# Performance work log

Hardware: AMD Instinct MI355X
Metric: run time of the kernel (lower is better)

Reference implementation:

```python
import jax, jax.numpy as jnp
import numpy as np

N, T, D_MODEL, H, DK = 4, 4096, 1024, 16, 64


def setup_inputs() -> dict:
    key = jax.random.key(0)
    ks = jax.random.split(key, 16)
    randn = lambda k, sh: jax.random.normal(k, sh, dtype=jnp.float32)
    # linear weights stored (in, out) so y = x @ W + b (math-equivalent to torch Linear)
    scale = 1.0 / np.sqrt(D_MODEL)
    return {
        "x_k": randn(ks[0], (N, T, D_MODEL)),
        "x_v": randn(ks[1], (N, T, D_MODEL)),
        "x_q": randn(ks[2], (N, T, D_MODEL)),
        "mask": jnp.ones((N, T), dtype=jnp.int32),
        "Wk": randn(ks[3], (D_MODEL, H * DK)) * scale,
        "bk": randn(ks[4], (H * DK,)) * 0.02,
        "Wv": randn(ks[5], (D_MODEL, H * DK)) * scale,
        "bv": randn(ks[6], (H * DK,)) * 0.02,
        "Wq": randn(ks[7], (D_MODEL, H * DK)) * scale,
        "bq": randn(ks[8], (H * DK,)) * 0.02,
        "alpha_w": randn(ks[9], (DK,)),
        "beta_w": randn(ks[10], (DK,)),
        "Wr": randn(ks[11], (DK, DK)) * (1.0 / np.sqrt(DK)),
        "br": randn(ks[12], (DK,)) * 0.02,
        "Wfc": randn(ks[13], (H * DK, D_MODEL)) * scale,
        "bfc": randn(ks[14], (D_MODEL,)) * 0.02,
    }


def _split_heads(x):  # (n, t, h*d) -> (n, h, t, d)
    n, t, _ = x.shape
    return x.reshape(n, t, H, DK).transpose(0, 2, 1, 3)


def reference(x_k, x_v, x_q, mask, Wk, bk, Wv, bv, Wq, bq,
              alpha_w, beta_w, Wr, br, Wfc, bfc):
    scale = DK ** (-0.5)
    k = _split_heads(x_k @ Wk + bk)  # (n, h, t, d)
    v = _split_heads(x_v @ Wv + bv)
    q = _split_heads(x_q @ Wq + bq)

    m = (mask == 0)[:, None, :]  # (n, 1, t) True where masked
    neg_inf = jnp.finfo(q.dtype).min

    # alpha pooling over queries -> global query (n, h, d)
    alpha = jnp.einsum('nhtd,d->nht', q, alpha_w) * scale
    alpha = jnp.where(m, neg_inf, alpha)
    alpha = jax.nn.softmax(alpha, axis=-1)
    global_query = jnp.einsum('nht,nhtd->nhd', alpha, q)

    # p = broadcast(global_query) * k, then beta pooling -> global key
    p = global_query[:, :, None, :] * k  # (n, h, t, d)
    beta = jnp.einsum('nhtd,d->nht', p, beta_w) * scale
    beta = jnp.where(m, neg_inf, beta)
    beta = jax.nn.softmax(beta, axis=-1)
    global_key = jnp.einsum('nht,nhtd->nhd', beta, p)

    u = global_key[:, :, None, :] * v  # (n, h, t, d)
    u_r = u @ Wr + br
    A = u_r + q  # (n, h, t, d)
    A = A.transpose(0, 2, 1, 3).reshape(N, T, H * DK)
    return A @ Wfc + bfc
```

## Files before the change

### kernel.cpp

```cpp
#include <hip/hip_runtime.h>

typedef __bf16 bf16x8 __attribute__((ext_vector_type(8)));
typedef float f32x4 __attribute__((ext_vector_type(4)));
typedef unsigned int u32x4 __attribute__((ext_vector_type(4)));
typedef unsigned short u16x4 __attribute__((ext_vector_type(4)));
typedef unsigned short u16x8 __attribute__((ext_vector_type(8)));

#define SEQ_T 4096
#define DMODEL 1024
#define HEADS 16
#define DKH 64
#define MTOK 16384

#define AS1 __attribute__((address_space(1)))
#define AS3 __attribute__((address_space(3)))

__device__ __forceinline__ unsigned short f2bf(float f) {
  unsigned u = __builtin_bit_cast(unsigned int, f);
  u += 0x7FFFu + ((u >> 16) & 1u);
  return (unsigned short)(u >> 16);
}
__device__ __forceinline__ float bf2f(unsigned short h) {
  unsigned u = ((unsigned)h) << 16;
  return __builtin_bit_cast(float, u);
}
__device__ __forceinline__ void gload16(const unsigned short* g, unsigned short* l) {
  __builtin_amdgcn_global_load_lds((const AS1 unsigned int*)(g),
                                   (AS3 unsigned int*)(l), 16, 0, 0);
}

__global__ void __launch_bounds__(256) k_cvt(const float* __restrict__ x,
                                             unsigned short* __restrict__ y,
                                             long long nelem) {
  long long i = ((long long)blockIdx.x * 256 + threadIdx.x) * 8;
  if (i >= nelem) return;
  u16x8 o;
#pragma unroll
  for (int j = 0; j < 8; ++j) o[j] = f2bf(x[i + j]);
  *(u16x8*)(y + i) = o;
}

__global__ void __launch_bounds__(256) k_wtrans(const float* __restrict__ W,
                                                unsigned short* __restrict__ Wt,
                                                int K, int N) {
  __shared__ float tile[32][33];
  int bn = blockIdx.x * 32, bk = blockIdx.y * 32;
  int tx = threadIdx.x, ty = threadIdx.y;
#pragma unroll
  for (int j = 0; j < 32; j += 8)
    tile[ty + j][tx] = W[(size_t)(bk + ty + j) * N + bn + tx];
  __syncthreads();
#pragma unroll
  for (int j = 0; j < 32; j += 8)
    Wt[(size_t)(bn + ty + j) * K + bk + tx] = f2bf(tile[tx][ty + j]);
}

#define BM 128
#define BN 128
#define BK 64

template <int OBF, int SCORE, int FUSEA>
__global__ void __launch_bounds__(256, 2)
k_gemm(const unsigned short* __restrict__ A, const unsigned short* __restrict__ Bt,
       const float* __restrict__ bias, void* __restrict__ C,
       const int* __restrict__ mask, const float* __restrict__ swt,
       float* __restrict__ sbuf, const unsigned short* __restrict__ qadd,
       int M, int N, int K) {
  __shared__ unsigned short As[BM * BK];
  __shared__ unsigned short Bs[BN * BK];
  const int tid = threadIdx.x;
  const int lane = tid & 63, wid = tid >> 6;
  const int wr = wid >> 1, wc = wid & 1;
  const int bnb = blockIdx.x;
  const int bm = blockIdx.y * BM, bn = bnb * BN;
  const int l15 = lane & 15, l4 = lane >> 4;

  const unsigned short* Btn = FUSEA ? Bt + ((size_t)(bm >> 12) << 20) : Bt;
  const float* biasn = FUSEA ? bias + ((bm >> 12) << 10) : bias;

  f32x4 acc[4][4];
#pragma unroll
  for (int i = 0; i < 4; ++i)
#pragma unroll
    for (int j = 0; j < 4; ++j)
#pragma unroll
      for (int e = 0; e < 4; ++e) acc[i][j][e] = 0.f;

  const int sgr = lane >> 3;
  const int sgc = (lane & 7) ^ sgr;

  for (int kt = 0; kt < K; kt += BK) {
    __syncthreads();
#pragma unroll
    for (int j = 0; j < 4; ++j) {
      int rb = wid * 32 + j * 8;
      gload16(A + (size_t)(bm + rb + sgr) * K + kt + sgc * 8, As + rb * BK);
    }
#pragma unroll
    for (int j = 0; j < 4; ++j) {
      int rb = wid * 32 + j * 8;
      gload16(Btn + (size_t)(bn + rb + sgr) * K + kt + sgc * 8, Bs + rb * BK);
    }
    __syncthreads();
#pragma unroll
    for (int kh = 0; kh < 2; ++kh) {
      bf16x8 af[4], bfr[4];
#pragma unroll
      for (int m = 0; m < 4; ++m) {
        int ra = wr * 64 + m * 16 + l15;
        int sl = (kh * 4 + l4) ^ (ra & 7);
        af[m] = *(const bf16x8*)(As + ra * BK + sl * 8);
      }
#pragma unroll
      for (int n = 0; n < 4; ++n) {
        int rb = wc * 64 + n * 16 + l15;
        int sl = (kh * 4 + l4) ^ (rb & 7);
        bfr[n] = *(const bf16x8*)(Bs + rb * BK + sl * 8);
      }
#pragma unroll
      for (int m = 0; m < 4; ++m)
#pragma unroll
        for (int n = 0; n < 4; ++n)
          acc[m][n] = __builtin_amdgcn_mfma_f32_16x16x32_bf16(af[m], bfr[n],
                                                              acc[m][n], 0, 0, 0);
    }
  }

  const int crow = bm + wr * 64 + l4 * 4;
  const int ccol = bn + wc * 64 + l15;

  float pacc[4][4];
  const float* wrow = nullptr;
  if (SCORE == 1) wrow = swt;
  if (SCORE) {
#pragma unroll
    for (int m = 0; m < 4; ++m)
#pragma unroll
      for (int e = 0; e < 4; ++e) pacc[m][e] = 0.f;
  }

#pragma unroll
  for (int m = 0; m < 4; ++m)
#pragma unroll
    for (int n = 0; n < 4; ++n) {
      int c = ccol + n * 16;
      float bj = biasn[c];
      float wg = SCORE ? wrow[n * 16 + l15] : 0.f;
#pragma unroll
      for (int e = 0; e < 4; ++e) {
        int r = crow + m * 16 + e;
        float v = acc[m][n][e] + bj;
        if (FUSEA) v += bf2f(qadd[(size_t)r * N + c]);
        if (SCORE) pacc[m][e] += v * wg;
        if (OBF)
          ((unsigned short*)C)[(size_t)r * N + c] = f2bf(v);
        else
          ((float*)C)[(size_t)r * N + c] = v;
      }
    }

  if (SCORE) {
#pragma unroll
    for (int m = 0; m < 4; ++m)
#pragma unroll
      for (int e = 0; e < 4; ++e) {
        float p = pacc[m][e];
        p += __shfl_xor(p, 1);
        p += __shfl_xor(p, 2);
        p += __shfl_xor(p, 4);
        p += __shfl_xor(p, 8);
        if (l15 == 0) {
          int r = crow + m * 16 + e;
          int t = r & (SEQ_T - 1), n = r >> 12;
          float sc = p * 0.125f;
          if (mask[n * SEQ_T + t] == 0) sc = -3.0e38f;
          sbuf[((size_t)n * HEADS + bnb * 2 + wc) * SEQ_T + t] = sc;
        }
      }
  }
}

__global__ void __launch_bounds__(256) k_softmax(const float* __restrict__ s,
                                                 float* __restrict__ mxo,
                                                 float* __restrict__ invo) {
  __shared__ float red[4];
  const int tid = threadIdx.x, lane = tid & 63, wid = tid >> 6;
  const float* sb = s + (size_t)blockIdx.x * SEQ_T;
  float m = -3.4e38f;
  for (int t = tid; t < SEQ_T; t += 256) m = fmaxf(m, sb[t]);
#pragma unroll
  for (int o = 1; o < 64; o <<= 1) m = fmaxf(m, __shfl_xor(m, o));
  if (lane == 0) red[wid] = m;
  __syncthreads();
  m = fmaxf(fmaxf(red[0], red[1]), fmaxf(red[2], red[3]));
  __syncthreads();
  float sum = 0.f;
  for (int t = tid; t < SEQ_T; t += 256) sum += __expf(sb[t] - m);
#pragma unroll
  for (int o = 1; o < 64; o <<= 1) sum += __shfl_xor(sum, o);
  if (lane == 0) red[wid] = sum;
  __syncthreads();
  if (tid == 0) {
    mxo[blockIdx.x] = m;
    invo[blockIdx.x] = 1.f / (red[0] + red[1] + red[2] + red[3]);
  }
}

__global__ void __launch_bounds__(256) k_wsum(const unsigned short* __restrict__ X,
                                              const float* __restrict__ s,
                                              const float* __restrict__ mxv,
                                              const float* __restrict__ invv,
                                              float* __restrict__ pbuf) {
  __shared__ float part[16][64];
  const int nh = blockIdx.x >> 4, chunk = blockIdx.x & 15;
  const int n = nh >> 4, h = nh & 15;
  const int tid = threadIdx.x, lane = tid & 63, wid = tid >> 6;
  const int tsub = lane >> 4, dl = lane & 15;
  const float mx = mxv[nh], inv = invv[nh];
  const float* sb = s + (size_t)nh * SEQ_T + chunk * 256;
  const size_t base = ((size_t)n * SEQ_T + chunk * 256) * DMODEL + h * DKH + dl * 4;
  f32x4 acc = {0.f, 0.f, 0.f, 0.f};
  for (int t = wid * 4 + tsub; t < 256; t += 16) {
    float w = __expf(sb[t] - mx) * inv;
    u16x4 xv = *(const u16x4*)(X + base + (size_t)t * DMODEL);
    acc[0] += w * bf2f(xv[0]);
    acc[1] += w * bf2f(xv[1]);
    acc[2] += w * bf2f(xv[2]);
    acc[3] += w * bf2f(xv[3]);
  }
  int g = wid * 4 + tsub;
#pragma unroll
  for (int e = 0; e < 4; ++e) part[g][dl * 4 + e] = acc[e];
  __syncthreads();
  if (tid < 64) {
    float v = 0.f;
#pragma unroll
    for (int gg = 0; gg < 16; ++gg) v += part[gg][tid];
    pbuf[(size_t)blockIdx.x * 64 + tid] = v;
  }
}

__global__ void __launch_bounds__(64) k_fin(const float* __restrict__ pbuf,
                                            const float* __restrict__ bw,
                                            float* __restrict__ out,
                                            float* __restrict__ wv) {
  const int nh = blockIdx.x, d = threadIdx.x;
  float v = 0.f;
#pragma unroll
  for (int c = 0; c < 16; ++c) v += pbuf[((size_t)nh * 16 + c) * 64 + d];
  out[(size_t)nh * 64 + d] = v;
  wv[(size_t)nh * 64 + d] = v * bw[d];
}

__global__ void __launch_bounds__(256) k_wksb(const float* __restrict__ Wk,
                                              const float* __restrict__ bk,
                                              const float* __restrict__ wv,
                                              unsigned short* __restrict__ WksT,
                                              float* __restrict__ bks) {
  const int nh = blockIdx.x, tid = threadIdx.x;
  const int n = nh >> 4, h = nh & 15;
  __shared__ float wvs[64];
  if (tid < 64) wvs[tid] = wv[(size_t)nh * 64 + tid];
  __syncthreads();
  int c0 = tid * 4;
  u16x4 o;
#pragma unroll
  for (int i = 0; i < 4; ++i) {
    int c = c0 + i;
    const float* wr = Wk + (size_t)c * DMODEL + h * DKH;
    float acc = 0.f;
#pragma unroll
    for (int dd = 0; dd < 64; dd += 4) {
      f32x4 w4 = *(const f32x4*)(wr + dd);
      acc += w4[0] * wvs[dd] + w4[1] * wvs[dd + 1] + w4[2] * wvs[dd + 2] +
             w4[3] * wvs[dd + 3];
    }
    o[i] = f2bf(acc);
  }
  *(u16x4*)(WksT + (size_t)n * 16 * DMODEL + (size_t)h * DMODEL + c0) = o;
  if (tid < 64) {
    float p = bk[h * 64 + tid] * wvs[tid];
#pragma unroll
    for (int ofs = 1; ofs < 64; ofs <<= 1) p += __shfl_xor(p, ofs);
    if (tid == 0) bks[nh] = p;
  }
}

__global__ void __launch_bounds__(128) k_score(const unsigned short* __restrict__ xk,
                                               const unsigned short* __restrict__ WksT,
                                               const float* __restrict__ bks,
                                               const int* __restrict__ mask,
                                               float* __restrict__ sbuf) {
  __shared__ unsigned short Xs[64 * 32];
  __shared__ unsigned short Ws[16 * 32];
  const int tid = threadIdx.x, lane = tid & 63, wid = tid >> 6;
  const int l15 = lane & 15, l4 = lane >> 4;
  const int bm = blockIdx.x * 64;
  const int n = bm >> 12;
  const unsigned short* Wn = WksT + (size_t)n * 16 * DMODEL;

  f32x4 acc[2];
#pragma unroll
  for (int m = 0; m < 2; ++m)
#pragma unroll
    for (int e = 0; e < 4; ++e) acc[m][e] = 0.f;

  const int srow = lane >> 2, scol = (lane & 3) * 8;
  for (int kt = 0; kt < DMODEL; kt += 32) {
    __syncthreads();
#pragma unroll
    for (int j = 0; j < 2; ++j) {
      int rb = wid * 32 + j * 16;
      gload16(xk + (size_t)(bm + rb + srow) * DMODEL + kt + scol, Xs + rb * 32);
    }
    if (wid == 0) gload16(Wn + (size_t)srow * DMODEL + kt + scol, Ws);
    __syncthreads();
    bf16x8 bfr = *(const bf16x8*)(Ws + l15 * 32 + l4 * 8);
#pragma unroll
    for (int m = 0; m < 2; ++m) {
      bf16x8 af = *(const bf16x8*)(Xs + (wid * 32 + m * 16 + l15) * 32 + l4 * 8);
      acc[m] = __builtin_amdgcn_mfma_f32_16x16x32_bf16(af, bfr, acc[m], 0, 0, 0);
    }
  }
  const int h = l15;
  const float bh = bks[n * 16 + h];
#pragma unroll
  for (int m = 0; m < 2; ++m)
#pragma unroll
    for (int e = 0; e < 4; ++e) {
      int r = bm + wid * 32 + m * 16 + l4 * 4 + e;
      int t = r & (SEQ_T - 1);
      float sc = (acc[m][e] + bh) * 0.125f;
      if (mask[n * SEQ_T + t] == 0) sc = -3.0e38f;
      sbuf[((size_t)n * HEADS + h) * SEQ_T + t] = sc;
    }
}

__global__ void __launch_bounds__(256) k_bwsum(const unsigned short* __restrict__ xk,
                                               const float* __restrict__ s,
                                               const float* __restrict__ smx,
                                               const float* __restrict__ sinv,
                                               float* __restrict__ part) {
  __shared__ float eb[16][64];
  const int tc = blockIdx.x, n = blockIdx.y, tid = threadIdx.x;
#pragma unroll
  for (int i = 0; i < 4; ++i) {
    int idx = i * 256 + tid;
    int h = idx >> 6, t = idx & 63;
    int nh = n * 16 + h;
    eb[h][t] = __expf(s[(size_t)nh * SEQ_T + tc * 64 + t] - smx[nh]) * sinv[nh];
  }
  __syncthreads();
  const int c0 = tid * 4;
  f32x4 acc[16];
#pragma unroll
  for (int h = 0; h < 16; ++h)
#pragma unroll
    for (int e = 0; e < 4; ++e) acc[h][e] = 0.f;
  const unsigned short* xb = xk + ((size_t)n * SEQ_T + tc * 64) * DMODEL + c0;
  for (int t = 0; t < 64; ++t) {
    u16x4 xr = *(const u16x4*)(xb + (size_t)t * DMODEL);
    float x0 = bf2f(xr[0]), x1 = bf2f(xr[1]), x2 = bf2f(xr[2]), x3 = bf2f(xr[3]);
#pragma unroll
    for (int h = 0; h < 16; ++h) {
      float w = eb[h][t];
      acc[h][0] += w * x0;
      acc[h][1] += w * x1;
      acc[h][2] += w * x2;
      acc[h][3] += w * x3;
    }
  }
#pragma unroll
  for (int h = 0; h < 16; ++h)
    *(f32x4*)(part + (((size_t)(n * 64 + tc)) * 16 + h) * DMODEL + c0) = acc[h];
}

__global__ void __launch_bounds__(256) k_gkr(const float* __restrict__ part,
                                             const unsigned short* __restrict__ WkT,
                                             const float* __restrict__ bk,
                                             const float* __restrict__ gq,
                                             float* __restrict__ gk) {
  __shared__ float pl[DMODEL];
  const int nh = blockIdx.x, tid = threadIdx.x;
  const int n = nh >> 4, h = nh & 15;
  const int c0 = tid * 4;
  f32x4 a4 = {0.f, 0.f, 0.f, 0.f};
  for (int tc = 0; tc < 64; ++tc) {
    f32x4 p = *(const f32x4*)(part + (((size_t)(n * 64 + tc)) * 16 + h) * DMODEL + c0);
    a4[0] += p[0]; a4[1] += p[1]; a4[2] += p[2]; a4[3] += p[3];
  }
#pragma unroll
  for (int e = 0; e < 4; ++e) pl[c0 + e] = a4[e];
  __syncthreads();
  if (tid < 64) {
    const unsigned short* wr = WkT + (size_t)(h * 64 + tid) * DMODEL;
    float acc = 0.f;
    for (int c = 0; c < DMODEL; c += 8) {
      u16x8 w = *(const u16x8*)(wr + c);
#pragma unroll
      for (int j = 0; j < 8; ++j) acc += pl[c + j] * bf2f(w[j]);
    }
    gk[(size_t)nh * 64 + tid] = gq[(size_t)nh * 64 + tid] * (acc + bk[h * 64 + tid]);
  }
}

__global__ void __launch_bounds__(256) k_wrgb(const float* __restrict__ gk,
                                              const float* __restrict__ Wr,
                                              const float* __restrict__ bv,
                                              const float* __restrict__ br,
                                              unsigned short* __restrict__ WrgT,
                                              float* __restrict__ bcomb) {
  __shared__ float wl[4096];
  const int nh = blockIdx.x, tid = threadIdx.x;
  const int n = nh >> 4, h = nh & 15;
#pragma unroll
  for (int i = 0; i < 16; ++i) {
    int idx = i * 256 + tid;
    int d = idx >> 6, dd = idx & 63;
    float v = gk[nh * 64 + dd] * Wr[dd * 64 + d];
    wl[idx] = v;
    WrgT[(size_t)nh * 4096 + idx] = f2bf(v);
  }
  __syncthreads();
  if (tid < 64) {
    float acc = br[tid];
#pragma unroll
    for (int dd = 0; dd < 64; ++dd) acc += bv[h * 64 + dd] * wl[tid * 64 + dd];
    bcomb[(size_t)n * DMODEL + h * 64 + tid] = acc;
  }
}

#define LDW 72
__global__ void __launch_bounds__(256) k_wcomb(const unsigned short* __restrict__ WrgT,
                                               const unsigned short* __restrict__ WvN,
                                               unsigned short* __restrict__ WcombT) {
  __shared__ unsigned short Wg[64 * LDW];
  __shared__ unsigned short Vv[128 * LDW];
  const int rc = blockIdx.x, nh = blockIdx.y;
  const int n = nh >> 4, h = nh & 15;
  const int tid = threadIdx.x, lane = tid & 63, wid = tid >> 6;
  const int l15 = lane & 15, l4 = lane >> 4;
#pragma unroll
  for (int i = 0; i < 2; ++i) {
    int v = i * 256 + tid;
    int d = v >> 3, k8 = v & 7;
    *(u16x8*)(Wg + d * LDW + k8 * 8) =
        *(const u16x8*)(WrgT + (size_t)nh * 4096 + d * 64 + k8 * 8);
  }
#pragma unroll
  for (int i = 0; i < 4; ++i) {
    int v = i * 256 + tid;
    int r = v >> 3, k8 = v & 7;
    *(u16x8*)(Vv + r * LDW + k8 * 8) =
        *(const u16x8*)(WvN + (size_t)(rc * 128 + r) * DMODEL + h * 64 + k8 * 8);
  }
  __syncthreads();
  f32x4 acc[8];
#pragma unroll
  for (int ct = 0; ct < 8; ++ct)
#pragma unroll
    for (int e = 0; e < 4; ++e) acc[ct][e] = 0.f;
#pragma unroll
  for (int ks = 0; ks < 2; ++ks) {
    bf16x8 af = *(const bf16x8*)(Wg + (wid * 16 + l15) * LDW + ks * 32 + l4 * 8);
#pragma unroll
    for (int ct = 0; ct < 8; ++ct) {
      bf16x8 bf = *(const bf16x8*)(Vv + (ct * 16 + l15) * LDW + ks * 32 + l4 * 8);
      acc[ct] = __builtin_amdgcn_mfma_f32_16x16x32_bf16(af, bf, acc[ct], 0, 0, 0);
    }
  }
  unsigned short* out = WcombT + ((size_t)n << 20);
#pragma unroll
  for (int ct = 0; ct < 8; ++ct)
#pragma unroll
    for (int e = 0; e < 4; ++e) {
      int d = h * 64 + wid * 16 + l4 * 4 + e;
      int r = rc * 128 + ct * 16 + l15;
      out[(size_t)d * DMODEL + r] = f2bf(acc[ct][e]);
    }
}

extern "C" void kernel_launch(void* const* d_in, const int* in_sizes, int n_in,
                              void* d_out, int out_size, void* d_ws, size_t ws_size,
                              hipStream_t stream) {
  const float* x_k = (const float*)d_in[0];
  const float* x_v = (const float*)d_in[1];
  const float* x_q = (const float*)d_in[2];
  const int* mask = (const int*)d_in[3];
  const float* Wk = (const float*)d_in[4];
  const float* bk = (const float*)d_in[5];
  const float* Wv = (const float*)d_in[6];
  const float* bv = (const float*)d_in[7];
  const float* Wq = (const float*)d_in[8];
  const float* bq = (const float*)d_in[9];
  const float* alpha_w = (const float*)d_in[10];
  const float* beta_w = (const float*)d_in[11];
  const float* Wr = (const float*)d_in[12];
  const float* br = (const float*)d_in[13];
  const float* Wfc = (const float*)d_in[14];
  const float* bfc = (const float*)d_in[15];

  unsigned short* qbf = (unsigned short*)d_out;

  char* ws = (char*)d_ws;
  const size_t MB = 1024 * 1024;
  unsigned short* xst = (unsigned short*)(ws);
  unsigned short* abuf = (unsigned short*)(ws + 32 * MB);
  unsigned short* WqT = (unsigned short*)(ws + 64 * MB);
  unsigned short* WkT = WqT + (size_t)DMODEL * DMODEL;
  unsigned short* WfT = WkT + (size_t)DMODEL * DMODEL;
  unsigned short* WvN = WfT + (size_t)DMODEL * DMODEL;
  unsigned short* WcombT = WvN + (size_t)DMODEL * DMODEL;
  unsigned short* WrgT = WcombT + (size_t)4 * DMODEL * DMODEL;
  unsigned short* WksT = WrgT + (size_t)64 * 4096;
  float* part = (float*)(WksT + (size_t)4 * 16 * DMODEL);
  float* pooled = part + (size_t)256 * 16 * DMODEL;
  float* sbuf = pooled + (size_t)64 * DMODEL;
  float* pbuf = sbuf + (size_t)64 * SEQ_T;
  float* smx = pbuf + 1024 * 64;
  float* sinv = smx + 64;
  float* gq = sinv + 64;
  float* wvb = gq + 4096;
  float* gk = wvb + 4096;
  float* bks = gk + 4096;
  float* bcomb = bks + 64;

  dim3 tb(32, 8);
  dim3 tg(DMODEL / 32, DMODEL / 32);
  k_wtrans<<<tg, tb, 0, stream>>>(Wq, WqT, DMODEL, DMODEL);
  k_wtrans<<<tg, tb, 0, stream>>>(Wk, WkT, DMODEL, DMODEL);
  k_wtrans<<<tg, tb, 0, stream>>>(Wfc, WfT, DMODEL, DMODEL);
  k_cvt<<<512, 256, 0, stream>>>(Wv, WvN, (long long)DMODEL * DMODEL);

  long long nx = (long long)MTOK * DMODEL;
  int cvtg = (int)(nx / 8 / 256);
  dim3 ggrid(DMODEL / BN, MTOK / BM);

  k_cvt<<<cvtg, 256, 0, stream>>>(x_q, xst, nx);
  k_gemm<1, 1, 0><<<ggrid, 256, 0, stream>>>(xst, WqT, bq, (void*)qbf, mask,
                                             alpha_w, sbuf, nullptr,
                                             MTOK, DMODEL, DMODEL);
  k_softmax<<<64, 256, 0, stream>>>(sbuf, smx, sinv);
  k_wsum<<<1024, 256, 0, stream>>>(qbf, sbuf, smx, sinv, pbuf);
  k_fin<<<64, 64, 0, stream>>>(pbuf, beta_w, gq, wvb);

  k_wksb<<<64, 256, 0, stream>>>(Wk, bk, wvb, WksT, bks);
  k_cvt<<<cvtg, 256, 0, stream>>>(x_k, xst, nx);
  k_score<<<MTOK / 64, 128, 0, stream>>>(xst, WksT, bks, mask, sbuf);
  k_softmax<<<64, 256, 0, stream>>>(sbuf, smx, sinv);
  dim3 bwg(64, 4);
  k_bwsum<<<bwg, 256, 0, stream>>>(xst, sbuf, smx, sinv, part);
  k_gkr<<<64, 256, 0, stream>>>(part, WkT, bk, gq, gk);

  k_wrgb<<<64, 256, 0, stream>>>(gk, Wr, bv, br, WrgT, bcomb);
  dim3 wcg(8, 64);
  k_wcomb<<<wcg, 256, 0, stream>>>(WrgT, WvN, WcombT);

  k_cvt<<<cvtg, 256, 0, stream>>>(x_v, xst, nx);
  k_gemm<1, 0, 1><<<ggrid, 256, 0, stream>>>(xst, WcombT, bcomb, (void*)abuf,
                                             nullptr, nullptr, nullptr, qbf,
                                             MTOK, DMODEL, DMODEL);

  k_gemm<0, 0, 0><<<ggrid, 256, 0, stream>>>(abuf, WfT, bfc, d_out, nullptr,
                                             nullptr, nullptr, nullptr,
                                             MTOK, DMODEL, DMODEL);
}
```

Before: 308.5 us.

## Merge input conversions, fuse tiny reduction kernels, and remap GEMM workgroup order

The three fp32-to-bf16 input conversions are merged into one launch that writes x_k into abuf and x_v into the second half of the output buffer. Two pairs of tiny kernels are fused (k_fin into k_wksb, and k_gkr with k_wrgb) so the global query and global key stay in shared memory instead of round-tripping through global memory. GEMM workgroups are remapped with a stride-8 permutation, likely to spread neighbouring tiles across XCDs for better L2 locality. The goal is fewer kernel launches and less global traffic. The cost is reusing the output buffer as scratch, which depends on the output being large enough.

```diff
diff --git a/kernel.cpp b/kernel.cpp
--- a/kernel.cpp
+++ b/kernel.cpp
@@ -34,6 +34,22 @@
                                              long long nelem) {
   long long i = ((long long)blockIdx.x * 256 + threadIdx.x) * 8;
   if (i >= nelem) return;
+  u16x8 o;
+#pragma unroll
+  for (int j = 0; j < 8; ++j) o[j] = f2bf(x[i + j]);
+  *(u16x8*)(y + i) = o;
+}
+
+__global__ void __launch_bounds__(256) k_cvt3(const float* __restrict__ xq,
+                                              const float* __restrict__ xk,
+                                              const float* __restrict__ xv,
+                                              unsigned short* __restrict__ oq,
+                                              unsigned short* __restrict__ ok,
+                                              unsigned short* __restrict__ ov) {
+  const int which = blockIdx.x >> 13;
+  const float* x = which == 0 ? xq : (which == 1 ? xk : xv);
+  unsigned short* y = which == 0 ? oq : (which == 1 ? ok : ov);
+  long long i = ((long long)(blockIdx.x & 8191) * 256 + threadIdx.x) * 8;
   u16x8 o;
 #pragma unroll
   for (int j = 0; j < 8; ++j) o[j] = f2bf(x[i + j]);
@@ -71,9 +87,13 @@
   const int tid = threadIdx.x;
   const int lane = tid & 63, wid = tid >> 6;
   const int wr = wid >> 1, wc = wid & 1;
-  const int bnb = blockIdx.x;
-  const int bm = blockIdx.y * BM, bn = bnb * BN;
   const int l15 = lane & 15, l4 = lane >> 4;
+
+  const int nwg = gridDim.x * gridDim.y;
+  const int flat = blockIdx.x + blockIdx.y * gridDim.x;
+  const int rm = (flat & 7) * (nwg >> 3) + (flat >> 3);
+  const int bx = rm % gridDim.x, by = rm / gridDim.x;
+  const int bm = by * BM, bn = bx * BN;
 
   const unsigned short* Btn = FUSEA ? Bt + ((size_t)(bm >> 12) << 20) : Bt;
   const float* biasn = FUSEA ? bias + ((bm >> 12) << 10) : bias;
@@ -174,7 +194,7 @@
           int t = r & (SEQ_T - 1), n = r >> 12;
           float sc = p * 0.125f;
           if (mask[n * SEQ_T + t] == 0) sc = -3.0e38f;
-          sbuf[((size_t)n * HEADS + bnb * 2 + wc) * SEQ_T + t] = sc;
+          sbuf[((size_t)n * HEADS + bx * 2 + wc) * SEQ_T + t] = sc;
         }
       }
   }
@@ -240,27 +260,23 @@
   }
 }
 
-__global__ void __launch_bounds__(64) k_fin(const float* __restrict__ pbuf,
-                                            const float* __restrict__ bw,
-                                            float* __restrict__ out,
-                                            float* __restrict__ wv) {
-  const int nh = blockIdx.x, d = threadIdx.x;
-  float v = 0.f;
-#pragma unroll
-  for (int c = 0; c < 16; ++c) v += pbuf[((size_t)nh * 16 + c) * 64 + d];
-  out[(size_t)nh * 64 + d] = v;
-  wv[(size_t)nh * 64 + d] = v * bw[d];
-}
-
 __global__ void __launch_bounds__(256) k_wksb(const float* __restrict__ Wk,
                                               const float* __restrict__ bk,
-                                              const float* __restrict__ wv,
+                                              const float* __restrict__ pbuf,
+                                              const float* __restrict__ bw,
+                                              float* __restrict__ gq,
                                               unsigned short* __restrict__ WksT,
                                               float* __restrict__ bks) {
   const int nh = blockIdx.x, tid = threadIdx.x;
   const int n = nh >> 4, h = nh & 15;
   __shared__ float wvs[64];
-  if (tid < 64) wvs[tid] = wv[(size_t)nh * 64 + tid];
+  if (tid < 64) {
+    float v = 0.f;
+#pragma unroll
+    for (int c = 0; c < 16; ++c) v += pbuf[((size_t)nh * 16 + c) * 64 + tid];
+    gq[(size_t)nh * 64 + tid] = v;
+    wvs[tid] = v * bw[tid];
+  }
   __syncthreads();
   int c0 = tid * 4;
   u16x4 o;
@@ -375,12 +391,18 @@
     *(f32x4*)(part + (((size_t)(n * 64 + tc)) * 16 + h) * DMODEL + c0) = acc[h];
 }
 
-__global__ void __launch_bounds__(256) k_gkr(const float* __restrict__ part,
-                                             const unsigned short* __restrict__ WkT,
-                                             const float* __restrict__ bk,
-                                             const float* __restrict__ gq,
-                                             float* __restrict__ gk) {
+__global__ void __launch_bounds__(256) k_gkrw(const float* __restrict__ part,
+                                              const unsigned short* __restrict__ WkT,
+                                              const float* __restrict__ bk,
+                                              const float* __restrict__ gq,
+                                              const float* __restrict__ Wr,
+                                              const float* __restrict__ bv,
+                                              const float* __restrict__ br,
+                                              unsigned short* __restrict__ WrgT,
+                                              float* __restrict__ bcomb) {
   __shared__ float pl[DMODEL];
+  __shared__ float gks[64];
+  __shared__ float wl[4096];
   const int nh = blockIdx.x, tid = threadIdx.x;
   const int n = nh >> 4, h = nh & 15;
   const int c0 = tid * 4;
@@ -400,24 +422,14 @@
 #pragma unroll
       for (int j = 0; j < 8; ++j) acc += pl[c + j] * bf2f(w[j]);
     }
-    gk[(size_t)nh * 64 + tid] = gq[(size_t)nh * 64 + tid] * (acc + bk[h * 64 + tid]);
-  }
-}
-
-__global__ void __launch_bounds__(256) k_wrgb(const float* __restrict__ gk,
-                                              const float* __restrict__ Wr,
-                                              const float* __restrict__ bv,
-                                              const float* __restrict__ br,
-                                              unsigned short* __restrict__ WrgT,
-                                              float* __restrict__ bcomb) {
-  __shared__ float wl[4096];
-  const int nh = blockIdx.x, tid = threadIdx.x;
-  const int n = nh >> 4, h = nh & 15;
+    gks[tid] = gq[(size_t)nh * 64 + tid] * (acc + bk[h * 64 + tid]);
+  }
+  __syncthreads();
 #pragma unroll
   for (int i = 0; i < 16; ++i) {
     int idx = i * 256 + tid;
     int d = idx >> 6, dd = idx & 63;
-    float v = gk[nh * 64 + dd] * Wr[dd * 64 + d];
+    float v = gks[dd] * Wr[dd * 64 + d];
     wl[idx] = v;
     WrgT[(size_t)nh * 4096 + idx] = f2bf(v);
   }
@@ -501,6 +513,7 @@
   const float* bfc = (const float*)d_in[15];
 
   unsigned short* qbf = (unsigned short*)d_out;
+  unsigned short* xvb = (unsigned short*)d_out + (size_t)MTOK * DMODEL;
 
   char* ws = (char*)d_ws;
   const size_t MB = 1024 * 1024;
@@ -514,15 +527,12 @@
   unsigned short* WrgT = WcombT + (size_t)4 * DMODEL * DMODEL;
   unsigned short* WksT = WrgT + (size_t)64 * 4096;
   float* part = (float*)(WksT + (size_t)4 * 16 * DMODEL);
-  float* pooled = part + (size_t)256 * 16 * DMODEL;
-  float* sbuf = pooled + (size_t)64 * DMODEL;
+  float* sbuf = part + (size_t)256 * 16 * DMODEL;
   float* pbuf = sbuf + (size_t)64 * SEQ_T;
   float* smx = pbuf + 1024 * 64;
   float* sinv = smx + 64;
   float* gq = sinv + 64;
-  float* wvb = gq + 4096;
-  float* gk = wvb + 4096;
-  float* bks = gk + 4096;
+  float* bks = gq + 4096;
   float* bcomb = bks + 64;
 
   dim3 tb(32, 8);
@@ -532,32 +542,27 @@
   k_wtrans<<<tg, tb, 0, stream>>>(Wfc, WfT, DMODEL, DMODEL);
   k_cvt<<<512, 256, 0, stream>>>(Wv, WvN, (long long)DMODEL * DMODEL);
 
-  long long nx = (long long)MTOK * DMODEL;
-  int cvtg = (int)(nx / 8 / 256);
+  k_cvt3<<<3 * 8192, 256, 0, stream>>>(x_q, x_k, x_v, xst, abuf, xvb);
+
   dim3 ggrid(DMODEL / BN, MTOK / BM);
 
-  k_cvt<<<cvtg, 256, 0, stream>>>(x_q, xst, nx);
   k_gemm<1, 1, 0><<<ggrid, 256, 0, stream>>>(xst, WqT, bq, (void*)qbf, mask,
                                              alpha_w, sbuf, nullptr,
                                              MTOK, DMODEL, DMODEL);
   k_softmax<<<64, 256, 0, stream>>>(sbuf, smx, sinv);
   k_wsum<<<1024, 256, 0, stream>>>(qbf, sbuf, smx, sinv, pbuf);
-  k_fin<<<64, 64, 0, stream>>>(pbuf, beta_w, gq, wvb);
-
-  k_wksb<<<64, 256, 0, stream>>>(Wk, bk, wvb, WksT, bks);
-  k_cvt<<<cvtg, 256, 0, stream>>>(x_k, xst, nx);
-  k_score<<<MTOK / 64, 128, 0, stream>>>(xst, WksT, bks, mask, sbuf);
+  k_wksb<<<64, 256, 0, stream>>>(Wk, bk, pbuf, beta_w, gq, WksT, bks);
+
+  k_score<<<MTOK / 64, 128, 0, stream>>>(abuf, WksT, bks, mask, sbuf);
   k_softmax<<<64, 256, 0, stream>>>(sbuf, smx, sinv);
   dim3 bwg(64, 4);
-  k_bwsum<<<bwg, 256, 0, stream>>>(xst, sbuf, smx, sinv, part);
-  k_gkr<<<64, 256, 0, stream>>>(part, WkT, bk, gq, gk);
-
-  k_wrgb<<<64, 256, 0, stream>>>(gk, Wr, bv, br, WrgT, bcomb);
+  k_bwsum<<<bwg, 256, 0, stream>>>(abuf, sbuf, smx, sinv, part);
+  k_gkrw<<<64, 256, 0, stream>>>(part, WkT, bk, gq, Wr, bv, br, WrgT, bcomb);
+
   dim3 wcg(8, 64);
   k_wcomb<<<wcg, 256, 0, stream>>>(WrgT, WvN, WcombT);
 
-  k_cvt<<<cvtg, 256, 0, stream>>>(x_v, xst, nx);
-  k_gemm<1, 0, 1><<<ggrid, 256, 0, stream>>>(xst, WcombT, bcomb, (void*)abuf,
+  k_gemm<1, 0, 1><<<ggrid, 256, 0, stream>>>(xvb, WcombT, bcomb, (void*)abuf,
                                              nullptr, nullptr, nullptr, qbf,
                                              MTOK, DMODEL, DMODEL);
 
```

New measurement: 280.8 us. 9.0% less time.
